# Kernel optimization log

Measured on AMD Instinct MI355X. Metric: run time of the kernel, lower is better.

Reference implementation:

```python
import jax, jax.numpy as jnp
import numpy as np

# Model dims (match init_kwargs)
D_MODEL = 768
EXPAND = 2
HEADDIM = 64
D_STATE = 64
D_CONV = 4
D_INNER = EXPAND * D_MODEL            # 1536 (== d_ssm, d_mlp = 0)
NHEADS = D_INNER // HEADDIM           # 24
CONV_DIM_PH = HEADDIM + 2 * D_STATE   # 192
CONV_DIM = NHEADS * CONV_DIM_PH       # 4608
D_IN_PROJ = D_INNER + CONV_DIM + NHEADS  # z + xBC + dt (d_mlp=0)

DT_MIN, DT_MAX = 1e-3, 1e-1


def setup_inputs() -> dict:
    key = jax.random.key(0)
    ks = jax.random.split(key, 12)
    B, L = 2, 2048
    s = 0.02
    # dt_bias init as in the torch module: inv_softplus of dt ~ loguniform(dt_min, dt_max)
    dt = jnp.exp(jax.random.uniform(ks[8], (NHEADS,)) * (np.log(DT_MAX) - np.log(DT_MIN)) + np.log(DT_MIN))
    dt = jnp.clip(dt, 1e-4, None)
    dt_bias = dt + jnp.log(-jnp.expm1(-dt))
    A_log = jnp.log(jax.random.uniform(ks[9], (NHEADS,), minval=1.0, maxval=16.0))
    return {
        "u": jax.random.normal(ks[0], (B, L, D_MODEL), jnp.float32),
        "W_in": jax.random.normal(ks[1], (D_IN_PROJ, D_MODEL), jnp.float32) * s,
        "conv_w": jax.random.normal(ks[2], (CONV_DIM, 1, D_CONV), jnp.float32) * 0.1,
        "conv_b": jnp.zeros((CONV_DIM,), jnp.float32),
        "R_x": jax.random.normal(ks[3], (NHEADS, HEADDIM, HEADDIM), jnp.float32) * 0.01,
        "R_B": jax.random.normal(ks[4], (NHEADS, D_STATE, HEADDIM), jnp.float32) * 0.01,
        "R_C": jax.random.normal(ks[5], (NHEADS, D_STATE, HEADDIM), jnp.float32) * 0.01,
        "R_dt": jax.random.normal(ks[6], (NHEADS, HEADDIM), jnp.float32) * 0.01,
        "dt_bias": dt_bias,
        "A_log": A_log,
        "D": jnp.ones((NHEADS, HEADDIM), jnp.float32),
        "W_out": jax.random.normal(ks[7], (D_MODEL, D_INNER), jnp.float32) * s,
    }


def reference(u, W_in, conv_w, conv_b, R_x, R_B, R_C, R_dt, dt_bias, A_log, D, W_out):
    B, L, _ = u.shape
    silu = jax.nn.silu

    # in_proj: split into SSM gate z, conv input xBC, dt pre-activation (d_mlp = 0)
    zxbcdt = u @ W_in.T                              # (B, L, D_IN_PROJ)
    z = zxbcdt[..., :D_INNER]                        # (B, L, d_ssm)
    xBC_in = zxbcdt[..., D_INNER:D_INNER + CONV_DIM] # (B, L, conv_dim)
    dt_raw = zxbcdt[..., D_INNER + CONV_DIM:]        # (B, L, NH)

    # causal depthwise conv1d (left-pad d_conv-1, truncate to L)
    xc = jax.lax.conv_general_dilated(
        xBC_in.transpose(0, 2, 1), conv_w,
        window_strides=(1,), padding=[(D_CONV - 1, 0)],
        dimension_numbers=("NCH", "OIH", "NCH"),
        feature_group_count=CONV_DIM) + conv_b[None, :, None]
    xBC_u = xc.transpose(0, 2, 1).reshape(B, L, NHEADS, CONV_DIM_PH)

    A = -jnp.exp(A_log)  # (NH,)

    def step(carry, inp):
        state, y_prev = carry            # (B,NH,DH,N), (B,NH,DH)
        xBC_t, dtr_t = inp               # (B,NH,DH+2N), (B,NH)
        x_u = xBC_t[..., :HEADDIM]
        B_u = xBC_t[..., HEADDIM:HEADDIM + D_STATE]
        C_u = xBC_t[..., HEADDIM + D_STATE:]
        # recurrent feedback of y_prev into x/B/C (pre-activation), then silu
        x = silu(x_u + jnp.einsum('hpq,bhq->bhp', R_x, y_prev))
        Bm = silu(B_u + jnp.einsum('hnq,bhq->bhn', R_B, y_prev))
        Cm = silu(C_u + jnp.einsum('hnq,bhq->bhn', R_C, y_prev))
        dt = jax.nn.softplus(dtr_t + jnp.einsum('hp,bhp->bh', R_dt, y_prev) + dt_bias)  # (B,NH)
        dA = jnp.exp(dt * A)             # (B,NH)
        state = state * dA[..., None, None] + (dt[..., None] * x)[..., None] * Bm[:, :, None, :]
        y = jnp.einsum('bhpn,bhn->bhp', state, Cm) + D * x   # (B,NH,DH)
        return (state, y), y

    state0 = jnp.zeros((B, NHEADS, HEADDIM, D_STATE), u.dtype)
    y0 = jnp.zeros((B, NHEADS, HEADDIM), u.dtype)
    xs = (xBC_u.transpose(1, 0, 2, 3), dt_raw.transpose(1, 0, 2))
    _, ys = jax.lax.scan(step, (state0, y0), xs)

    y = ys.transpose(1, 0, 2, 3)                              # (B,L,NH,DH)
    y = y * silu(z.reshape(B, L, NHEADS, HEADDIM))            # SSM gating
    out = y.reshape(B, L, D_INNER) @ W_out.T                  # (B,L,d_model)
    return out
```

## Files before the change

### kernel.cpp

```cpp
#include <hip/hip_runtime.h>

#define B_SZ    2
#define LSEQ    2048
#define DMODEL  768
#define DINNER  1536
#define NHEADS  24
#define HD      64
#define CDPH    192
#define CONVDIM 4608
#define DIP     6168
#define MROWS   (B_SZ*LSEQ)

typedef float f2 __attribute__((ext_vector_type(2)));
typedef float f32x4 __attribute__((ext_vector_type(4)));
typedef short bf16x8 __attribute__((ext_vector_type(8)));

__device__ __forceinline__ float siluf(float x) {
    return x / (1.0f + __expf(-x));
}

#define WBAR() do { asm volatile("s_waitcnt lgkmcnt(0)" ::: "memory"); \
                    __builtin_amdgcn_s_barrier();                      \
                    asm volatile("" ::: "memory"); } while (0)

__device__ __forceinline__ float redux4(float v) {
    float o = __int_as_float(
        __builtin_amdgcn_ds_swizzle(__float_as_int(v), 0x401F));
    float s = v + o;
    float a = s, b = s;
    asm("v_permlane32_swap_b32 %0, %1" : "+v"(a), "+v"(b));
    return a + b;
}

__device__ __forceinline__ ushort f2bf(float v) {
    uint u = __float_as_uint(v);
    return (ushort)((u + 0x7FFFu + ((u >> 16) & 1u)) >> 16);
}
__device__ __forceinline__ float bf2f(ushort h) {
    return __uint_as_float(((uint)h) << 16);
}

__global__ __launch_bounds__(256) void gemm_nt_split(
    const float* __restrict__ A, const float* __restrict__ B,
    float* __restrict__ C, int M, int N, int K)
{
    __shared__ ushort As_hi[128][56];
    __shared__ ushort As_lo[128][56];
    __shared__ ushort Bs_hi[128][56];
    __shared__ ushort Bs_lo[128][56];

    const int ntn = (N + 127) >> 7;
    const int bm = blockIdx.x / ntn;
    const int bn = blockIdx.x - bm * ntn;
    const int m0 = bm << 7, n0 = bn << 7;
    const int tid = threadIdx.x;
    const int wid = tid >> 6;
    const int l = tid & 63;
    const int wm = wid >> 1, wn = wid & 1;
    const int lr = l & 15;
    const int kq = l >> 4;

    const int srow = tid >> 1;
    const int scol = (tid & 1) << 4;
    const float* Ap = A + (size_t)(m0 + srow) * K + scol;
    const bool bok = (n0 + srow) < N;
    const float* Bp = B + (size_t)(n0 + srow) * K + scol;

    f32x4 acc[4][4];
#pragma unroll
    for (int i = 0; i < 4; ++i)
#pragma unroll
        for (int j = 0; j < 4; ++j) acc[i][j] = f32x4{0.f, 0.f, 0.f, 0.f};

    for (int k0 = 0; k0 < K; k0 += 32) {
        float av[16], bv[16];
#pragma unroll
        for (int q = 0; q < 4; ++q) {
            const float4 t = *(const float4*)(Ap + k0 + q * 4);
            av[q*4+0] = t.x; av[q*4+1] = t.y; av[q*4+2] = t.z; av[q*4+3] = t.w;
        }
#pragma unroll
        for (int q = 0; q < 4; ++q) {
            float4 t = make_float4(0.f, 0.f, 0.f, 0.f);
            if (bok) t = *(const float4*)(Bp + k0 + q * 4);
            bv[q*4+0] = t.x; bv[q*4+1] = t.y; bv[q*4+2] = t.z; bv[q*4+3] = t.w;
        }
        __syncthreads();
#pragma unroll
        for (int q = 0; q < 16; ++q) {
            const ushort ah = f2bf(av[q]);
            As_hi[srow][scol + q] = ah;
            As_lo[srow][scol + q] = f2bf(av[q] - bf2f(ah));
            const ushort bh = f2bf(bv[q]);
            Bs_hi[srow][scol + q] = bh;
            Bs_lo[srow][scol + q] = f2bf(bv[q] - bf2f(bh));
        }
        __syncthreads();

        bf16x8 ah[4], al[4], bh[4], bl[4];
#pragma unroll
        for (int f = 0; f < 4; ++f) {
            const int ra = wm * 64 + f * 16 + lr;
            ah[f] = *(const bf16x8*)&As_hi[ra][kq * 8];
            al[f] = *(const bf16x8*)&As_lo[ra][kq * 8];
            const int rb = wn * 64 + f * 16 + lr;
            bh[f] = *(const bf16x8*)&Bs_hi[rb][kq * 8];
            bl[f] = *(const bf16x8*)&Bs_lo[rb][kq * 8];
        }
#pragma unroll
        for (int i = 0; i < 4; ++i)
#pragma unroll
            for (int j = 0; j < 4; ++j) {
                acc[i][j] = __builtin_amdgcn_mfma_f32_16x16x32_bf16(
                    ah[i], bh[j], acc[i][j], 0, 0, 0);
                acc[i][j] = __builtin_amdgcn_mfma_f32_16x16x32_bf16(
                    ah[i], bl[j], acc[i][j], 0, 0, 0);
                acc[i][j] = __builtin_amdgcn_mfma_f32_16x16x32_bf16(
                    al[i], bh[j], acc[i][j], 0, 0, 0);
            }
    }

#pragma unroll
    for (int i = 0; i < 4; ++i) {
#pragma unroll
        for (int j = 0; j < 4; ++j) {
            const int n = n0 + wn * 64 + j * 16 + lr;
            if (n < N) {
#pragma unroll
                for (int rg = 0; rg < 4; ++rg) {
                    const int m = m0 + wm * 64 + i * 16 + kq * 4 + rg;
                    C[(size_t)m * N + n] = acc[i][j][rg];
                }
            }
        }
    }
}

__global__ __launch_bounds__(512, 1) void mamba_scan6(
    const float* __restrict__ zx,
    const float* __restrict__ conv_w,
    const float* __restrict__ conv_b,
    const float* __restrict__ R_x,
    const float* __restrict__ R_B,
    const float* __restrict__ R_C,
    const float* __restrict__ R_dt,
    const float* __restrict__ dt_bias,
    const float* __restrict__ A_log,
    const float* __restrict__ Dvec,
    float* __restrict__ yz)
{
    const int tid = threadIdx.x;
    const int ch = tid >> 8;
    const int bh = blockIdx.x * 2 + ch;
    const int b = bh / NHEADS;
    const int h = bh % NHEADS;
    const int w = (tid >> 6) & 3;
    const int l = tid & 63;
    const int g = l >> 4;
    const int r = l & 15;
    const int p = (w << 4) + r;

    __shared__ __attribute__((aligned(16))) float ybuf[2][64];
    __shared__ __attribute__((aligned(16))) float Bml[2][64];
    __shared__ __attribute__((aligned(16))) float Cml[2][64];

    f2 Rx2[8], Rb2[8], Rc2[8], Rd2[8];
    {
        const size_t ro = ((size_t)h * 64 + p) * 64 + (g << 4);
#pragma unroll
        for (int q = 0; q < 4; ++q) {
            const float4 v = *(const float4*)(R_x + ro + q * 4);
            Rx2[q*2] = f2{v.x, v.y}; Rx2[q*2+1] = f2{v.z, v.w};
        }
#pragma unroll
        for (int q = 0; q < 4; ++q) {
            const float4 v = *(const float4*)(R_B + ro + q * 4);
            Rb2[q*2] = f2{v.x, v.y}; Rb2[q*2+1] = f2{v.z, v.w};
        }
#pragma unroll
        for (int q = 0; q < 4; ++q) {
            const float4 v = *(const float4*)(R_C + ro + q * 4);
            Rc2[q*2] = f2{v.x, v.y}; Rc2[q*2+1] = f2{v.z, v.w};
        }
#pragma unroll
        for (int q = 0; q < 4; ++q) {
            const float4 v = *(const float4*)(R_dt + h * 64 + (g << 4) + q * 4);
            Rd2[q*2] = f2{v.x, v.y}; Rd2[q*2+1] = f2{v.z, v.w};
        }
    }
    const float Aval = -__expf(A_log[h]);
    const float bias = dt_bias[h];
    const float Dp   = Dvec[h * 64 + p];

    float wx0, wx1, wx2, wx3, wb0, wb1, wb2, wb3, wc0, wc1, wc2, wc3;
    float cbx, cbB, cbC;
    {
        const float* cw = conv_w + (size_t)h * CDPH * 4;
        const float4 vx = *(const float4*)(cw + (size_t)p * 4);
        const float4 vb = *(const float4*)(cw + (size_t)(64 + p) * 4);
        const float4 vc = *(const float4*)(cw + (size_t)(128 + p) * 4);
        wx0 = vx.x; wx1 = vx.y; wx2 = vx.z; wx3 = vx.w;
        wb0 = vb.x; wb1 = vb.y; wb2 = vb.z; wb3 = vb.w;
        wc0 = vc.x; wc1 = vc.y; wc2 = vc.z; wc3 = vc.w;
        cbx = conv_b[h * CDPH + p];
        cbB = conv_b[h * CDPH + 64 + p];
        cbC = conv_b[h * CDPH + 128 + p];
    }
    float hx0 = 0.f, hx1 = 0.f, hx2 = 0.f;
    float hB0 = 0.f, hB1 = 0.f, hB2 = 0.f;
    float hC0 = 0.f, hC1 = 0.f, hC2 = 0.f;

    const float* xbc = zx + (size_t)b * LSEQ * DIP + DINNER + h * CDPH;
    const float* zb  = zx + (size_t)b * LSEQ * DIP + h * HD;
    const float* dtp = zx + (size_t)b * LSEQ * DIP + DINNER + CONVDIM + h;
    float* yzb = yz + (size_t)b * LSEQ * DINNER + h * HD;

    f2 st2[8];
#pragma unroll
    for (int q = 0; q < 8; ++q) st2[q] = f2{0.f, 0.f};

    if (g == 0) ybuf[ch][p] = 0.f;
    __syncthreads();

    float vx_c = xbc[p], vB_c = xbc[64 + p], vC_c = xbc[128 + p];
    float z_c = zb[p];
    float dtr_c = dtp[0];

    for (int t = 0; t < LSEQ; ++t) {
        const float xcx = fmaf(wx3, vx_c, fmaf(wx2, hx2, fmaf(wx1, hx1, fmaf(wx0, hx0, cbx))));
        const float xcB = fmaf(wb3, vB_c, fmaf(wb2, hB2, fmaf(wb1, hB1, fmaf(wb0, hB0, cbB))));
        const float xcC = fmaf(wc3, vC_c, fmaf(wc2, hC2, fmaf(wc1, hC1, fmaf(wc0, hC0, cbC))));
        hx0 = hx1; hx1 = hx2; hx2 = vx_c;
        hB0 = hB1; hB1 = hB2; hB2 = vB_c;
        hC0 = hC1; hC1 = hC2; hC2 = vC_c;

        const size_t roff = (size_t)((t + 1 < LSEQ) ? t + 1 : t) * DIP;
        const float vx_n = xbc[roff + p];
        const float vB_n = xbc[roff + 64 + p];
        const float vC_n = xbc[roff + 128 + p];
        const float z_n  = zb[roff + p];
        const float dtr_n = dtp[roff];

        const float4* yb4 = (const float4*)(&ybuf[ch][g << 4]);
        f2 ax2 = {0.f, 0.f}, ab2 = {0.f, 0.f}, ac2 = {0.f, 0.f}, ad2 = {0.f, 0.f};
#pragma unroll
        for (int qq = 0; qq < 4; ++qq) {
            const float4 y4 = yb4[qq];
            const f2 ylo = {y4.x, y4.y}, yhi = {y4.z, y4.w};
            ax2 += Rx2[qq*2] * ylo; ax2 += Rx2[qq*2+1] * yhi;
            ab2 += Rb2[qq*2] * ylo; ab2 += Rb2[qq*2+1] * yhi;
            ac2 += Rc2[qq*2] * ylo; ac2 += Rc2[qq*2+1] * yhi;
            ad2 += Rd2[qq*2] * ylo; ad2 += Rd2[qq*2+1] * yhi;
        }
        const float ax = ax2.x + ax2.y, ab = ab2.x + ab2.y;
        const float ac = ac2.x + ac2.y, ad = ad2.x + ad2.y;

        const float Bm = siluf(xcB + redux4(ab));
        const float Cm = siluf(xcC + redux4(ac));
        if (g == 0) { Bml[ch][p] = Bm; Cml[ch][p] = Cm; }
        WBAR();

        const float4* bm4 = (const float4*)(&Bml[ch][g << 4]);
        const float4* cm4 = (const float4*)(&Cml[ch][g << 4]);
        const float4 bA = bm4[0], bB = bm4[1], bC = bm4[2], bD = bm4[3];
        const float4 cA = cm4[0], cB = cm4[1], cC = cm4[2], cD = cm4[3];

        const float xv = siluf(xcx + redux4(ax));
        const float dv = dtr_c + redux4(ad) + bias;
        const float dtv = (dv > 15.f) ? dv : __logf(1.f + __expf(dv));
        const float dAv = __expf(dtv * Aval);
        const float kx = dtv * xv;
        const float zg = siluf(z_c);

        const f2 dA2 = {dAv, dAv};
        const f2 kx2 = {kx, kx};
        f2 bmv[8], cmv[8];
        bmv[0] = f2{bA.x, bA.y}; bmv[1] = f2{bA.z, bA.w};
        bmv[2] = f2{bB.x, bB.y}; bmv[3] = f2{bB.z, bB.w};
        bmv[4] = f2{bC.x, bC.y}; bmv[5] = f2{bC.z, bC.w};
        bmv[6] = f2{bD.x, bD.y}; bmv[7] = f2{bD.z, bD.w};
        cmv[0] = f2{cA.x, cA.y}; cmv[1] = f2{cA.z, cA.w};
        cmv[2] = f2{cB.x, cB.y}; cmv[3] = f2{cB.z, cB.w};
        cmv[4] = f2{cC.x, cC.y}; cmv[5] = f2{cC.z, cC.w};
        cmv[6] = f2{cD.x, cD.y}; cmv[7] = f2{cD.z, cD.w};
        f2 yp2 = {0.f, 0.f};
#pragma unroll
        for (int q = 0; q < 8; ++q) {
            st2[q] = st2[q] * dA2 + kx2 * bmv[q];
            yp2 += st2[q] * cmv[q];
        }
        float yp = yp2.x + yp2.y;
        yp = redux4(yp);
        const float ynew = yp + Dp * xv;

        if (g == 0) {
            ybuf[ch][p] = ynew;
            yzb[(size_t)t * DINNER + p] = ynew * zg;
        }
        WBAR();

        vx_c = vx_n; vB_c = vB_n; vC_c = vC_n; z_c = z_n; dtr_c = dtr_n;
    }
}

extern "C" void kernel_launch(void* const* d_in, const int* in_sizes, int n_in,
                              void* d_out, int out_size, void* d_ws, size_t ws_size,
                              hipStream_t stream) {
    const float* u       = (const float*)d_in[0];
    const float* W_in    = (const float*)d_in[1];
    const float* conv_w  = (const float*)d_in[2];
    const float* conv_b  = (const float*)d_in[3];
    const float* R_x     = (const float*)d_in[4];
    const float* R_B     = (const float*)d_in[5];
    const float* R_C     = (const float*)d_in[6];
    const float* R_dt    = (const float*)d_in[7];
    const float* dt_bias = (const float*)d_in[8];
    const float* A_log   = (const float*)d_in[9];
    const float* Dv      = (const float*)d_in[10];
    const float* W_out   = (const float*)d_in[11];
    float* out = (float*)d_out;

    float* zx = (float*)d_ws;
    float* yz = zx + (size_t)MROWS * DIP;

    {
        const int M = MROWS, N = DIP, K = DMODEL;
        const int grid = (M / 128) * ((N + 127) / 128);
        gemm_nt_split<<<grid, 256, 0, stream>>>(u, W_in, zx, M, N, K);
    }
    mamba_scan6<<<(B_SZ * NHEADS) / 2, 512, 0, stream>>>(
        zx, conv_w, conv_b, R_x, R_B, R_C, R_dt, dt_bias, A_log, Dv, yz);
    {
        const int M = MROWS, N = DMODEL, K = DINNER;
        const int grid = (M / 128) * ((N + 127) / 128);
        gemm_nt_split<<<grid, 256, 0, stream>>>(yz, W_out, out, M, N, K);
    }
}
```

Measured before the change: 2.326 ms.

## Use one head per 256-thread block and a permlane-based reduction in the scan

The recurrent scan kernel now gives each (batch, head) pair its own 256-thread block instead of packing two pairs into a 512-thread block. Each per-step barrier then spans 4 waves instead of 8, and twice as many blocks run across the CUs. The 4-lane reduction replaces the LDS-backed ds_swizzle with v_permlane16_swap, cutting per-step latency on the serial critical path. The gate silu is computed earlier and addressing uses incremented pointers; the prefetch is no longer clamped, so the last iteration reads one row past each batch's data (still inside the workspace) and discards it.

```diff
diff --git a/kernel.cpp b/kernel.cpp
--- a/kernel.cpp
+++ b/kernel.cpp
@@ -24,12 +24,12 @@
                     asm volatile("" ::: "memory"); } while (0)
 
 __device__ __forceinline__ float redux4(float v) {
-    float o = __int_as_float(
-        __builtin_amdgcn_ds_swizzle(__float_as_int(v), 0x401F));
-    float s = v + o;
-    float a = s, b = s;
-    asm("v_permlane32_swap_b32 %0, %1" : "+v"(a), "+v"(b));
-    return a + b;
+    float a = v, b = v;
+    asm("v_permlane16_swap_b32 %0, %1" : "+v"(a), "+v"(b));
+    const float s = a + b;
+    float c = s, d = s;
+    asm("v_permlane32_swap_b32 %0, %1" : "+v"(c), "+v"(d));
+    return c + d;
 }
 
 __device__ __forceinline__ ushort f2bf(float v) {
@@ -136,7 +136,7 @@
     }
 }
 
-__global__ __launch_bounds__(512, 1) void mamba_scan6(
+__global__ __launch_bounds__(256, 1) void mamba_scan7(
     const float* __restrict__ zx,
     const float* __restrict__ conv_w,
     const float* __restrict__ conv_b,
@@ -149,20 +149,18 @@
     const float* __restrict__ Dvec,
     float* __restrict__ yz)
 {
+    const int b = blockIdx.x / NHEADS;
+    const int h = blockIdx.x % NHEADS;
     const int tid = threadIdx.x;
-    const int ch = tid >> 8;
-    const int bh = blockIdx.x * 2 + ch;
-    const int b = bh / NHEADS;
-    const int h = bh % NHEADS;
-    const int w = (tid >> 6) & 3;
+    const int w = tid >> 6;
     const int l = tid & 63;
     const int g = l >> 4;
     const int r = l & 15;
     const int p = (w << 4) + r;
 
-    __shared__ __attribute__((aligned(16))) float ybuf[2][64];
-    __shared__ __attribute__((aligned(16))) float Bml[2][64];
-    __shared__ __attribute__((aligned(16))) float Cml[2][64];
+    __shared__ __attribute__((aligned(16))) float ybuf[64];
+    __shared__ __attribute__((aligned(16))) float Bml[64];
+    __shared__ __attribute__((aligned(16))) float Cml[64];
 
     f2 Rx2[8], Rb2[8], Rc2[8], Rd2[8];
     {
@@ -219,12 +217,13 @@
 #pragma unroll
     for (int q = 0; q < 8; ++q) st2[q] = f2{0.f, 0.f};
 
-    if (g == 0) ybuf[ch][p] = 0.f;
+    if (g == 0) ybuf[p] = 0.f;
     __syncthreads();
 
     float vx_c = xbc[p], vB_c = xbc[64 + p], vC_c = xbc[128 + p];
     float z_c = zb[p];
     float dtr_c = dtp[0];
+    int off = DIP;
 
     for (int t = 0; t < LSEQ; ++t) {
         const float xcx = fmaf(wx3, vx_c, fmaf(wx2, hx2, fmaf(wx1, hx1, fmaf(wx0, hx0, cbx))));
@@ -234,14 +233,14 @@
         hB0 = hB1; hB1 = hB2; hB2 = vB_c;
         hC0 = hC1; hC1 = hC2; hC2 = vC_c;
 
-        const size_t roff = (size_t)((t + 1 < LSEQ) ? t + 1 : t) * DIP;
-        const float vx_n = xbc[roff + p];
-        const float vB_n = xbc[roff + 64 + p];
-        const float vC_n = xbc[roff + 128 + p];
-        const float z_n  = zb[roff + p];
-        const float dtr_n = dtp[roff];
-
-        const float4* yb4 = (const float4*)(&ybuf[ch][g << 4]);
+        const float vx_n = xbc[off + p];
+        const float vB_n = xbc[off + 64 + p];
+        const float vC_n = xbc[off + 128 + p];
+        const float z_n  = zb[off + p];
+        const float dtr_n = dtp[off];
+        const float zg = siluf(z_c);
+
+        const float4* yb4 = (const float4*)(ybuf + (g << 4));
         f2 ax2 = {0.f, 0.f}, ab2 = {0.f, 0.f}, ac2 = {0.f, 0.f}, ad2 = {0.f, 0.f};
 #pragma unroll
         for (int qq = 0; qq < 4; ++qq) {
@@ -257,11 +256,11 @@
 
         const float Bm = siluf(xcB + redux4(ab));
         const float Cm = siluf(xcC + redux4(ac));
-        if (g == 0) { Bml[ch][p] = Bm; Cml[ch][p] = Cm; }
+        if (g == 0) { Bml[p] = Bm; Cml[p] = Cm; }
         WBAR();
 
-        const float4* bm4 = (const float4*)(&Bml[ch][g << 4]);
-        const float4* cm4 = (const float4*)(&Cml[ch][g << 4]);
+        const float4* bm4 = (const float4*)(Bml + (g << 4));
+        const float4* cm4 = (const float4*)(Cml + (g << 4));
         const float4 bA = bm4[0], bB = bm4[1], bC = bm4[2], bD = bm4[3];
         const float4 cA = cm4[0], cB = cm4[1], cC = cm4[2], cD = cm4[3];
 
@@ -270,7 +269,6 @@
         const float dtv = (dv > 15.f) ? dv : __logf(1.f + __expf(dv));
         const float dAv = __expf(dtv * Aval);
         const float kx = dtv * xv;
-        const float zg = siluf(z_c);
 
         const f2 dA2 = {dAv, dAv};
         const f2 kx2 = {kx, kx};
@@ -289,17 +287,17 @@
             st2[q] = st2[q] * dA2 + kx2 * bmv[q];
             yp2 += st2[q] * cmv[q];
         }
-        float yp = yp2.x + yp2.y;
-        yp = redux4(yp);
-        const float ynew = yp + Dp * xv;
+        const float ynew = redux4(yp2.x + yp2.y) + Dp * xv;
 
         if (g == 0) {
-            ybuf[ch][p] = ynew;
-            yzb[(size_t)t * DINNER + p] = ynew * zg;
+            ybuf[p] = ynew;
+            yzb[p] = ynew * zg;
         }
         WBAR();
 
         vx_c = vx_n; vB_c = vB_n; vC_c = vC_n; z_c = z_n; dtr_c = dtr_n;
+        off += DIP;
+        yzb += DINNER;
     }
 }
 
@@ -328,7 +326,7 @@
         const int grid = (M / 128) * ((N + 127) / 128);
         gemm_nt_split<<<grid, 256, 0, stream>>>(u, W_in, zx, M, N, K);
     }
-    mamba_scan6<<<(B_SZ * NHEADS) / 2, 512, 0, stream>>>(
+    mamba_scan7<<<B_SZ * NHEADS, 256, 0, stream>>>(
         zx, conv_w, conv_b, R_x, R_B, R_C, R_dt, dt_bias, A_log, Dv, yz);
     {
         const int M = MROWS, N = DMODEL, K = DINNER;
```

After: 2.002 ms. 13.9% less time.
